# Optimization experiments

Hardware: AMD Instinct MI355X
Metric: run time of the kernel (lower is better)

Reference implementation:

```python
import jax, jax.numpy as jnp
import numpy as np

N = 100000       # num nodes
E = 1600000      # num edges (avg degree 16)
IN, HID, OUT, C = 128, 64, 64, 16


def setup_inputs() -> dict:
    key = jax.random.key(0)
    ks = jax.random.split(key, 10)
    x = jax.random.normal(ks[0], (N, IN), jnp.float32)
    edge_index = jax.random.randint(ks[1], (2, E), 0, N, dtype=jnp.int32)
    dict_node = jax.random.randint(ks[2], (N,), 0, N, dtype=jnp.int32)
    # learned parameters (Glorot-ish scaling)
    W1 = jax.random.normal(ks[3], (IN, HID), jnp.float32) / np.sqrt(IN)
    b1 = jnp.zeros((HID,), jnp.float32)
    W2 = jax.random.normal(ks[4], (HID, OUT), jnp.float32) / np.sqrt(HID)
    b2 = jnp.zeros((OUT,), jnp.float32)
    Wfc = jax.random.normal(ks[5], (OUT, C), jnp.float32) / np.sqrt(OUT)
    bfc = jnp.zeros((C,), jnp.float32)
    return {"x": x, "edge_index": edge_index, "dict_node": dict_node,
            "W1": W1, "b1": b1, "W2": W2, "b2": b2, "Wfc": Wfc, "bfc": bfc}


def _gcn_conv(h_in, W, b, src, dst, n):
    """GCNConv: D^-1/2 (A+I) D^-1/2 (X W) + b, self-loops handled analytically."""
    h = h_in @ W                                   # [N, F]
    deg = jax.ops.segment_sum(jnp.ones((src.shape[0],), h.dtype), dst,
                              num_segments=n) + 1.0  # +1 self-loop
    dinv = jax.lax.rsqrt(deg)                      # [N]
    norm = dinv[src] * dinv[dst]                   # [E]
    agg = jax.ops.segment_sum(h[src] * norm[:, None], dst, num_segments=n)
    agg = agg + h * (dinv * dinv)[:, None]         # self-loop contribution
    return agg + b


def reference(x, edge_index, dict_node, W1, b1, W2, b2, Wfc, bfc):
    n = x.shape[0]
    src, dst = edge_index[0], edge_index[1]
    h = jax.nn.relu(_gcn_conv(x, W1, b1, src, dst, n))
    # dropout p=0.5 is identity at inference
    h = jax.nn.relu(_gcn_conv(h, W2, b2, src, dst, n))
    # global_mean_pool over dict_node with size = num_nodes
    cnt = jax.ops.segment_sum(jnp.ones((n,), h.dtype), dict_node, num_segments=n)
    summ = jax.ops.segment_sum(h, dict_node, num_segments=n)
    pooled = summ / jnp.maximum(cnt, 1.0)[:, None]
    logits = pooled @ Wfc + bfc
    return jax.nn.log_softmax(logits, axis=1)
```

## Files before the change

kernel.cpp:

```cpp
#include <hip/hip_runtime.h>

#define THREADS 256
#define KC 32
#define B1 256

__device__ inline ushort f2bf(float v) {
    union { float f; unsigned u; } a; a.f = v;
    unsigned r = a.u + 0x7fff + ((a.u >> 16) & 1);
    return (ushort)(r >> 16);
}
__device__ inline unsigned pack2(float a, float b) {
    return (unsigned)f2bf(a) | ((unsigned)f2bf(b) << 16);
}
__device__ inline float bflo(unsigned v) {
    union { unsigned u; float f; } a; a.u = v << 16; return a.f;
}
__device__ inline float bfhi(unsigned v) {
    union { unsigned u; float f; } a; a.u = v & 0xffff0000u; return a.f;
}


__global__ void k_p1(const int* __restrict__ dst, int* __restrict__ pc,
                     int E, int NB, int chunk) {
    __shared__ int hist[512];
    int tid = threadIdx.x, blk = blockIdx.x;
    for (int i = tid; i < NB; i += THREADS) hist[i] = 0;
    __syncthreads();
    int e0 = blk * chunk;
    int e1 = e0 + chunk; if (e1 > E) e1 = E;
    for (int e = e0 + tid; e < e1; e += THREADS)
        atomicAdd(&hist[dst[e] >> 8], 1);
    __syncthreads();
    for (int i = tid; i < NB; i += THREADS) pc[i * B1 + blk] = hist[i];
}

__global__ void k_s1(int* __restrict__ pc, int* __restrict__ bsums, int total) {
    __shared__ int s[1024];
    int t = threadIdx.x;
    int idx = blockIdx.x * 1024 + t;
    int v = (idx < total) ? pc[idx] : 0;
    s[t] = v;
    __syncthreads();
    for (int o = 1; o < 1024; o <<= 1) {
        int x = (t >= (unsigned)o) ? s[t - o] : 0;
        __syncthreads();
        s[t] += x;
        __syncthreads();
    }
    if (idx < total) pc[idx] = s[t] - v;
    if (t == 1023) bsums[blockIdx.x] = s[1023];
}

__global__ void k_s2(int* __restrict__ bsums, int nb) {
    __shared__ int s[128];
    int t = threadIdx.x;
    int v = (t < nb) ? bsums[t] : 0;
    s[t] = v;
    __syncthreads();
    for (int o = 1; o < 128; o <<= 1) {
        int x = (t >= (unsigned)o) ? s[t - o] : 0;
        __syncthreads();
        s[t] += x;
        __syncthreads();
    }
    if (t < nb) bsums[t] = s[t] - v;
}


__global__ void k_p2(const int* __restrict__ src, const int* __restrict__ dst,
                     const int* __restrict__ pc, const int* __restrict__ bsx,
                     unsigned long long* __restrict__ part, int E, int NB, int chunk) {
    __shared__ int cur[512];
    int tid = threadIdx.x, blk = blockIdx.x;
    for (int i = tid; i < NB; i += THREADS) {
        int idx = i * B1 + blk;
        cur[i] = pc[idx] + bsx[idx >> 10];
    }
    __syncthreads();
    int e0 = blk * chunk;
    int e1 = e0 + chunk; if (e1 > E) e1 = E;
    for (int e = e0 + tid; e < e1; e += THREADS) {
        int d = dst[e], sv = src[e];
        int pos = atomicAdd(&cur[d >> 8], 1);
        part[pos] = ((unsigned long long)(unsigned)d << 32) | (unsigned)sv;
    }
}

__global__ void k_p3(const unsigned long long* __restrict__ part,
                     const int* __restrict__ pc, const int* __restrict__ bsx,
                     int* __restrict__ off, float* __restrict__ dinv,
                     int* __restrict__ csr, int E, int NB, int n) {
    __shared__ int hist[256];
    __shared__ int so[256];
    int b = blockIdx.x, t = threadIdx.x;
    int i0 = b * B1, i1 = (b + 1) * B1;
    int base = pc[i0] + bsx[i0 >> 10];
    int end  = (b + 1 < NB) ? (pc[i1] + bsx[i1 >> 10]) : E;
    hist[t] = 0;
    __syncthreads();
    for (int e = base + t; e < end; e += THREADS)
        atomicAdd(&hist[(int)(part[e] >> 32) & 255], 1);
    __syncthreads();
    int h = hist[t];
    so[t] = h;
    __syncthreads();
    for (int o = 1; o < 256; o <<= 1) {
        int x = (t >= (unsigned)o) ? so[t - o] : 0;
        __syncthreads();
        so[t] += x;
        __syncthreads();
    }
    int ex = so[t] - h;
    int node = (b << 8) + t;
    if (node < n) {
        off[node]  = base + ex;
        dinv[node] = rsqrtf((float)h + 1.0f);
        if (node == n - 1) off[n] = E;
    }
    __syncthreads();
    so[t] = base + ex;
    __syncthreads();
    for (int e = base + t; e < end; e += THREADS) {
        unsigned long long p = part[e];
        int pos = atomicAdd(&so[(int)(p >> 32) & 255], 1);
        csr[pos] = (int)(p & 0xffffffffu);
    }
}

__global__ __launch_bounds__(THREADS) void
k_g1(const float* __restrict__ X, const float* __restrict__ W,
     const float* __restrict__ dinv, ushort* __restrict__ C, int n, int fin,
     const int* __restrict__ dict, float* __restrict__ cnt, int nGemm, int nCnt) {
    int tid = threadIdx.x;
    if ((int)blockIdx.x >= nGemm) {
        int stride = nCnt * THREADS;
        for (int i = ((int)blockIdx.x - nGemm) * THREADS + tid; i < n; i += stride)
            atomicAdd(&cnt[dict[i]], 1.0f);
        return;
    }
    __shared__ float Xs[KC][68];
    __shared__ float Ws[KC][64];
    int r0  = blockIdx.x * 64;
    int tx4 = (tid & 15) * 4;
    int ty4 = (tid >> 4) * 4;
    int sxr = tid >> 2, sxk = (tid & 3) * 4;
    int swk = tid >> 4, swc = (tid & 15) * 4;
    int xrow = r0 + sxr; if (xrow >= n) xrow = n - 1;
    const float* xptr = X + (size_t)xrow * fin;
    float4 acc0 = {0,0,0,0}, acc1 = {0,0,0,0}, acc2 = {0,0,0,0}, acc3 = {0,0,0,0};
    for (int kc = 0; kc < fin; kc += KC) {
        float4 xa = *(const float4*)(xptr + kc + sxk);
        float4 xb = *(const float4*)(xptr + kc + 16 + sxk);
        float4 wa = *(const float4*)(W + (size_t)(kc + swk) * 64 + swc);
        float4 wb = *(const float4*)(W + (size_t)(kc + swk + 16) * 64 + swc);
        __syncthreads();
        Xs[sxk + 0][sxr] = xa.x; Xs[sxk + 1][sxr] = xa.y;
        Xs[sxk + 2][sxr] = xa.z; Xs[sxk + 3][sxr] = xa.w;
        Xs[16 + sxk + 0][sxr] = xb.x; Xs[16 + sxk + 1][sxr] = xb.y;
        Xs[16 + sxk + 2][sxr] = xb.z; Xs[16 + sxk + 3][sxr] = xb.w;
        *(float4*)&Ws[swk][swc]      = wa;
        *(float4*)&Ws[swk + 16][swc] = wb;
        __syncthreads();
        #pragma unroll 8
        for (int k = 0; k < KC; ++k) {
            float4 a = *(const float4*)&Xs[k][ty4];
            float4 b = *(const float4*)&Ws[k][tx4];
            acc0.x = fmaf(a.x, b.x, acc0.x); acc0.y = fmaf(a.x, b.y, acc0.y);
            acc0.z = fmaf(a.x, b.z, acc0.z); acc0.w = fmaf(a.x, b.w, acc0.w);
            acc1.x = fmaf(a.y, b.x, acc1.x); acc1.y = fmaf(a.y, b.y, acc1.y);
            acc1.z = fmaf(a.y, b.z, acc1.z); acc1.w = fmaf(a.y, b.w, acc1.w);
            acc2.x = fmaf(a.z, b.x, acc2.x); acc2.y = fmaf(a.z, b.y, acc2.y);
            acc2.z = fmaf(a.z, b.z, acc2.z); acc2.w = fmaf(a.z, b.w, acc2.w);
            acc3.x = fmaf(a.w, b.x, acc3.x); acc3.y = fmaf(a.w, b.y, acc3.y);
            acc3.z = fmaf(a.w, b.z, acc3.z); acc3.w = fmaf(a.w, b.w, acc3.w);
        }
    }
    int row = r0 + ty4;
    #pragma unroll
    for (int r = 0; r < 4; ++r) {
        if (row + r >= n) break;
        float dn = dinv[row + r];
        float4 a = r == 0 ? acc0 : r == 1 ? acc1 : r == 2 ? acc2 : acc3;
        ushort4 o;
        o.x = f2bf(a.x * dn); o.y = f2bf(a.y * dn);
        o.z = f2bf(a.z * dn); o.w = f2bf(a.w * dn);
        *(ushort4*)(C + (size_t)(row + r) * 64 + tx4) = o;
    }
}

__global__ __launch_bounds__(THREADS) void
k_gemm_bf16(const ushort* __restrict__ X, const float* __restrict__ W,
            const float* __restrict__ dinv, ushort* __restrict__ C, int n, int fin) {
    __shared__ float Xs[KC][68];
    __shared__ float Ws[KC][64];
    int tid = threadIdx.x;
    int r0  = blockIdx.x * 64;
    int tx4 = (tid & 15) * 4;
    int ty4 = (tid >> 4) * 4;
    int sxr = tid >> 2, sk8 = (tid & 3) * 8;
    int swk = tid >> 4, swc = (tid & 15) * 4;
    int xrow = r0 + sxr; if (xrow >= n) xrow = n - 1;
    const ushort* xptr = X + (size_t)xrow * fin;
    float4 acc0 = {0,0,0,0}, acc1 = {0,0,0,0}, acc2 = {0,0,0,0}, acc3 = {0,0,0,0};
    for (int kc = 0; kc < fin; kc += KC) {
        uint4 xv = *(const uint4*)(xptr + kc + sk8);
        float4 wa = *(const float4*)(W + (size_t)(kc + swk) * 64 + swc);
        float4 wb = *(const float4*)(W + (size_t)(kc + swk + 16) * 64 + swc);
        __syncthreads();
        Xs[sk8 + 0][sxr] = bflo(xv.x); Xs[sk8 + 1][sxr] = bfhi(xv.x);
        Xs[sk8 + 2][sxr] = bflo(xv.y); Xs[sk8 + 3][sxr] = bfhi(xv.y);
        Xs[sk8 + 4][sxr] = bflo(xv.z); Xs[sk8 + 5][sxr] = bfhi(xv.z);
        Xs[sk8 + 6][sxr] = bflo(xv.w); Xs[sk8 + 7][sxr] = bfhi(xv.w);
        *(float4*)&Ws[swk][swc]      = wa;
        *(float4*)&Ws[swk + 16][swc] = wb;
        __syncthreads();
        #pragma unroll 8
        for (int k = 0; k < KC; ++k) {
            float4 a = *(const float4*)&Xs[k][ty4];
            float4 b = *(const float4*)&Ws[k][tx4];
            acc0.x = fmaf(a.x, b.x, acc0.x); acc0.y = fmaf(a.x, b.y, acc0.y);
            acc0.z = fmaf(a.x, b.z, acc0.z); acc0.w = fmaf(a.x, b.w, acc0.w);
            acc1.x = fmaf(a.y, b.x, acc1.x); acc1.y = fmaf(a.y, b.y, acc1.y);
            acc1.z = fmaf(a.y, b.z, acc1.z); acc1.w = fmaf(a.y, b.w, acc1.w);
            acc2.x = fmaf(a.z, b.x, acc2.x); acc2.y = fmaf(a.z, b.y, acc2.y);
            acc2.z = fmaf(a.z, b.z, acc2.z); acc2.w = fmaf(a.z, b.w, acc2.w);
            acc3.x = fmaf(a.w, b.x, acc3.x); acc3.y = fmaf(a.w, b.y, acc3.y);
            acc3.z = fmaf(a.w, b.z, acc3.z); acc3.w = fmaf(a.w, b.w, acc3.w);
        }
    }
    int row = r0 + ty4;
    #pragma unroll
    for (int r = 0; r < 4; ++r) {
        if (row + r >= n) break;
        float dn = dinv[row + r];
        float4 a = r == 0 ? acc0 : r == 1 ? acc1 : r == 2 ? acc2 : acc3;
        ushort4 o;
        o.x = f2bf(a.x * dn); o.y = f2bf(a.y * dn);
        o.z = f2bf(a.z * dn); o.w = f2bf(a.w * dn);
        *(ushort4*)(C + (size_t)(row + r) * 64 + tx4) = o;
    }
}

__device__ inline void gather_sum8(const ushort* __restrict__ H,
                                   const int* __restrict__ csr,
                                   int node, int j, int end, int g, int q,
                                   float4& R0, float4& R1) {
    float4 A0 = {0,0,0,0}, B0 = {0,0,0,0}, A1 = {0,0,0,0}, B1v = {0,0,0,0};
    if (g == 0) {
        uint4 sv = *(const uint4*)(H + ((size_t)node << 6) + q * 8);
        A0.x += bflo(sv.x); A0.y += bfhi(sv.x); A0.z += bflo(sv.y); A0.w += bfhi(sv.y);
        B0.x += bflo(sv.z); B0.y += bfhi(sv.z); B0.z += bflo(sv.w); B0.w += bfhi(sv.w);
    }
    for (; j + 16 <= end; j += 16) {
        int s0 = csr[j + g];
        int s1 = csr[j + 8 + g];
        uint4 v0 = *(const uint4*)(H + ((size_t)s0 << 6) + q * 8);
        uint4 v1 = *(const uint4*)(H + ((size_t)s1 << 6) + q * 8);
        A0.x += bflo(v0.x); A0.y += bfhi(v0.x); A0.z += bflo(v0.y); A0.w += bfhi(v0.y);
        B0.x += bflo(v0.z); B0.y += bfhi(v0.z); B0.z += bflo(v0.w); B0.w += bfhi(v0.w);
        A1.x += bflo(v1.x); A1.y += bfhi(v1.x); A1.z += bflo(v1.y); A1.w += bfhi(v1.y);
        B1v.x += bflo(v1.z); B1v.y += bfhi(v1.z); B1v.z += bflo(v1.w); B1v.w += bfhi(v1.w);
    }
    if (j + 8 <= end) {
        int s0 = csr[j + g];
        uint4 v0 = *(const uint4*)(H + ((size_t)s0 << 6) + q * 8);
        A0.x += bflo(v0.x); A0.y += bfhi(v0.x); A0.z += bflo(v0.y); A0.w += bfhi(v0.y);
        B0.x += bflo(v0.z); B0.y += bfhi(v0.z); B0.z += bflo(v0.w); B0.w += bfhi(v0.w);
        j += 8;
    }
    if (g < end - j) {
        int s1 = csr[j + g];
        uint4 v1 = *(const uint4*)(H + ((size_t)s1 << 6) + q * 8);
        A1.x += bflo(v1.x); A1.y += bfhi(v1.x); A1.z += bflo(v1.y); A1.w += bfhi(v1.y);
        B1v.x += bflo(v1.z); B1v.y += bfhi(v1.z); B1v.z += bflo(v1.w); B1v.w += bfhi(v1.w);
    }
    R0.x = A0.x + A1.x; R0.y = A0.y + A1.y; R0.z = A0.z + A1.z; R0.w = A0.w + A1.w;
    R1.x = B0.x + B1v.x; R1.y = B0.y + B1v.y; R1.z = B0.z + B1v.z; R1.w = B0.w + B1v.w;
    #pragma unroll
    for (int o = 8; o <= 32; o <<= 1) {
        R0.x += __shfl_xor(R0.x, o); R0.y += __shfl_xor(R0.y, o);
        R0.z += __shfl_xor(R0.z, o); R0.w += __shfl_xor(R0.w, o);
        R1.x += __shfl_xor(R1.x, o); R1.y += __shfl_xor(R1.y, o);
        R1.z += __shfl_xor(R1.z, o); R1.w += __shfl_xor(R1.w, o);
    }
}

__global__ void k_gcn_gather(const ushort* __restrict__ H, const int* __restrict__ csr,
                             const int* __restrict__ off, const float* __restrict__ dinv,
                             const float* __restrict__ b, ushort* __restrict__ out, int n) {
    int t = blockIdx.x * blockDim.x + threadIdx.x;
    int node = t >> 6;
    if (node >= n) return;
    int lane = threadIdx.x & 63;
    int g = lane >> 3, q = lane & 7;
    float4 R0, R1;
    gather_sum8(H, csr, node, off[node], off[node + 1], g, q, R0, R1);
    if (g == 0) {
        float dn = dinv[node];
        float4 b0 = *(const float4*)(b + q * 8);
        float4 b1 = *(const float4*)(b + q * 8 + 4);
        float v0 = R0.x * dn + b0.x, v1 = R0.y * dn + b0.y;
        float v2 = R0.z * dn + b0.z, v3 = R0.w * dn + b0.w;
        float v4 = R1.x * dn + b1.x, v5 = R1.y * dn + b1.y;
        float v6 = R1.z * dn + b1.z, v7 = R1.w * dn + b1.w;
        uint4 o;
        o.x = pack2(v0 > 0.f ? v0 : 0.f, v1 > 0.f ? v1 : 0.f);
        o.y = pack2(v2 > 0.f ? v2 : 0.f, v3 > 0.f ? v3 : 0.f);
        o.z = pack2(v4 > 0.f ? v4 : 0.f, v5 > 0.f ? v5 : 0.f);
        o.w = pack2(v6 > 0.f ? v6 : 0.f, v7 > 0.f ? v7 : 0.f);
        *(uint4*)(out + ((size_t)node << 6) + q * 8) = o;
    }
}

__global__ void k_gcn_gather_fc(const ushort* __restrict__ H, const int* __restrict__ csr,
                                const int* __restrict__ off, const float* __restrict__ dinv,
                                const float* __restrict__ b, const float* __restrict__ Wfc,
                                const int* __restrict__ dict, float* __restrict__ pool16,
                                int n) {
    __shared__ float wt[16 * 65];
    __shared__ float hrow[4][64];
    int tid = threadIdx.x;
    for (int i = tid; i < 64 * 16; i += THREADS) {
        int cc = i >> 4, r = i & 15;
        wt[r * 65 + cc] = Wfc[i];
    }
    __syncthreads();
    int t = blockIdx.x * blockDim.x + tid;
    int node = t >> 6;
    int lane = tid & 63;
    int g = lane >> 3, q = lane & 7;
    int nl = tid >> 6;
    if (node < n) {
        float4 R0, R1;
        gather_sum8(H, csr, node, off[node], off[node + 1], g, q, R0, R1);
        if (g == 0) {
            float dn = dinv[node];
            float4 b0 = *(const float4*)(b + q * 8);
            float4 b1 = *(const float4*)(b + q * 8 + 4);
            float4 v0, v1;
            v0.x = R0.x * dn + b0.x; v0.y = R0.y * dn + b0.y;
            v0.z = R0.z * dn + b0.z; v0.w = R0.w * dn + b0.w;
            v1.x = R1.x * dn + b1.x; v1.y = R1.y * dn + b1.y;
            v1.z = R1.z * dn + b1.z; v1.w = R1.w * dn + b1.w;
            v0.x = v0.x > 0.f ? v0.x : 0.f; v0.y = v0.y > 0.f ? v0.y : 0.f;
            v0.z = v0.z > 0.f ? v0.z : 0.f; v0.w = v0.w > 0.f ? v0.w : 0.f;
            v1.x = v1.x > 0.f ? v1.x : 0.f; v1.y = v1.y > 0.f ? v1.y : 0.f;
            v1.z = v1.z > 0.f ? v1.z : 0.f; v1.w = v1.w > 0.f ? v1.w : 0.f;
            *(float4*)&hrow[nl][q * 8]     = v0;
            *(float4*)&hrow[nl][q * 8 + 4] = v1;
        }
        int g2 = lane >> 4, r = lane & 15;
        float p = 0.f;
        #pragma unroll
        for (int i = 0; i < 16; ++i) {
            int cc = g2 * 16 + i;
            p = fmaf(hrow[nl][cc], wt[r * 65 + cc], p);
        }
        p += __shfl_xor(p, 16);
        p += __shfl_xor(p, 32);
        if (g2 == 0)
            atomicAdd(&pool16[(size_t)dict[node] * 16 + r], p);
    }
}

__global__ void k_final16(const float* __restrict__ pool16, const float* __restrict__ cnt,
                          const float* __restrict__ bfc, float* __restrict__ out, int n) {
    int tid = threadIdx.x;
    int nl = tid >> 4, lane = tid & 15;
    int node = blockIdx.x * 16 + nl;
    if (node >= n) return;
    float inv = 1.0f / fmaxf(cnt[node], 1.0f);
    float acc = pool16[(size_t)node * 16 + lane] * inv + bfc[lane];
    float m = acc;
    for (int o = 8; o; o >>= 1) m = fmaxf(m, __shfl_xor(m, o, 16));
    float ex = __expf(acc - m);
    float s = ex;
    for (int o = 8; o; o >>= 1) s += __shfl_xor(s, o, 16);
    out[(size_t)node * 16 + lane] = acc - m - __logf(s);
}

extern "C" void kernel_launch(void* const* d_in, const int* in_sizes, int n_in,
                              void* d_out, int out_size, void* d_ws, size_t ws_size,
                              hipStream_t stream) {
    const float* x    = (const float*)d_in[0];
    const int*   ei   = (const int*)d_in[1];
    const int*   dict = (const int*)d_in[2];
    const float* W1   = (const float*)d_in[3];
    const float* b1   = (const float*)d_in[4];
    const float* W2   = (const float*)d_in[5];
    const float* b2   = (const float*)d_in[6];
    const float* Wfc  = (const float*)d_in[7];
    const float* bfc  = (const float*)d_in[8];

    const int N  = in_sizes[2];
    const int E  = in_sizes[1] / 2;
    const int IN = in_sizes[0] / N;
    const int* src = ei;
    const int* dst = ei + E;

    ushort* bufA = (ushort*)d_ws;
    ushort* bufB = bufA + (size_t)N * 64;
    unsigned long long* part = (unsigned long long*)bufB;
    float* dinv    = (float*)(bufB + (size_t)N * 64);
    float* cnt     = dinv + N;
    int*   off     = (int*)(cnt + N);
    int*   pcounts = off + (N + 1);
    const int NB     = (N + 255) >> 8;
    const int pcsize = NB * B1;
    int*   bsums   = pcounts + pcsize;
    int*   csr     = bsums + 128;
    float* pool16  = (float*)(csr + E);

    const int gNE   = (N * 64 + THREADS - 1) / THREADS;
    const int gTile = (N + 63) / 64;
    const int gRows = (N + 15) / 16;
    const int nCnt  = 256;
    const int chunk = (E + B1 - 1) / B1;
    const int nS1   = (pcsize + 1023) >> 10;

    hipMemsetAsync(cnt, 0, (size_t)N * sizeof(float), stream);
    hipMemsetAsync(pool16, 0, (size_t)N * 16 * sizeof(float), stream);

    k_p1<<<B1, THREADS, 0, stream>>>(dst, pcounts, E, NB, chunk);
    k_s1<<<nS1, 1024, 0, stream>>>(pcounts, bsums, pcsize);
    k_s2<<<1, 128, 0, stream>>>(bsums, nS1);
    k_p2<<<B1, THREADS, 0, stream>>>(src, dst, pcounts, bsums, part, E, NB, chunk);
    k_p3<<<NB, THREADS, 0, stream>>>(part, pcounts, bsums, off, dinv, csr, E, NB, N);

    k_g1<<<gTile + nCnt, THREADS, 0, stream>>>(x, W1, dinv, bufA, N, IN,
                                               dict, cnt, gTile, nCnt);

    k_gcn_gather<<<gNE, THREADS, 0, stream>>>(bufA, csr, off, dinv, b1, bufB, N);

    k_gemm_bf16<<<gTile, THREADS, 0, stream>>>(bufB, W2, dinv, bufA, N, 64);
    k_gcn_gather_fc<<<gNE, THREADS, 0, stream>>>(bufA, csr, off, dinv, b2, Wfc,
                                                 dict, pool16, N);

    k_final16<<<gRows, THREADS, 0, stream>>>(pool16, cnt, bfc, (float*)d_out, N);
}
```

Baseline: 312.9 us.

## Aggregate neighbor features with MFMA segment-sum over 16-node groups per wavefront

```diff
diff --git a/kernel.cpp b/kernel.cpp
--- a/kernel.cpp
+++ b/kernel.cpp
@@ -3,6 +3,10 @@
 #define THREADS 256
 #define KC 32
 #define B1 256
+
+typedef __attribute__((ext_vector_type(8))) short bf16x8;
+typedef __attribute__((ext_vector_type(4))) float f32x4;
+typedef __attribute__((ext_vector_type(2))) unsigned int u32x2;
 
 __device__ inline ushort f2bf(float v) {
     union { float f; unsigned u; } a; a.f = v;
@@ -65,7 +69,6 @@
     }
     if (t < nb) bsums[t] = s[t] - v;
 }
-
 
 __global__ void k_p2(const int* __restrict__ src, const int* __restrict__ dst,
                      const int* __restrict__ pc, const int* __restrict__ bsx,
@@ -241,125 +244,166 @@
     }
 }
 
-__device__ inline void gather_sum8(const ushort* __restrict__ H,
-                                   const int* __restrict__ csr,
-                                   int node, int j, int end, int g, int q,
-                                   float4& R0, float4& R1) {
-    float4 A0 = {0,0,0,0}, B0 = {0,0,0,0}, A1 = {0,0,0,0}, B1v = {0,0,0,0};
-    if (g == 0) {
-        uint4 sv = *(const uint4*)(H + ((size_t)node << 6) + q * 8);
-        A0.x += bflo(sv.x); A0.y += bfhi(sv.x); A0.z += bflo(sv.y); A0.w += bfhi(sv.y);
-        B0.x += bflo(sv.z); B0.y += bfhi(sv.z); B0.z += bflo(sv.w); B0.w += bfhi(sv.w);
-    }
-    for (; j + 16 <= end; j += 16) {
-        int s0 = csr[j + g];
-        int s1 = csr[j + 8 + g];
-        uint4 v0 = *(const uint4*)(H + ((size_t)s0 << 6) + q * 8);
-        uint4 v1 = *(const uint4*)(H + ((size_t)s1 << 6) + q * 8);
-        A0.x += bflo(v0.x); A0.y += bfhi(v0.x); A0.z += bflo(v0.y); A0.w += bfhi(v0.y);
-        B0.x += bflo(v0.z); B0.y += bfhi(v0.z); B0.z += bflo(v0.w); B0.w += bfhi(v0.w);
-        A1.x += bflo(v1.x); A1.y += bfhi(v1.x); A1.z += bflo(v1.y); A1.w += bfhi(v1.y);
-        B1v.x += bflo(v1.z); B1v.y += bfhi(v1.z); B1v.z += bflo(v1.w); B1v.w += bfhi(v1.w);
-    }
-    if (j + 8 <= end) {
-        int s0 = csr[j + g];
-        uint4 v0 = *(const uint4*)(H + ((size_t)s0 << 6) + q * 8);
-        A0.x += bflo(v0.x); A0.y += bfhi(v0.x); A0.z += bflo(v0.y); A0.w += bfhi(v0.y);
-        B0.x += bflo(v0.z); B0.y += bfhi(v0.z); B0.z += bflo(v0.w); B0.w += bfhi(v0.w);
-        j += 8;
-    }
-    if (g < end - j) {
-        int s1 = csr[j + g];
-        uint4 v1 = *(const uint4*)(H + ((size_t)s1 << 6) + q * 8);
-        A1.x += bflo(v1.x); A1.y += bfhi(v1.x); A1.z += bflo(v1.y); A1.w += bfhi(v1.y);
-        B1v.x += bflo(v1.z); B1v.y += bfhi(v1.z); B1v.z += bflo(v1.w); B1v.w += bfhi(v1.w);
-    }
-    R0.x = A0.x + A1.x; R0.y = A0.y + A1.y; R0.z = A0.z + A1.z; R0.w = A0.w + A1.w;
-    R1.x = B0.x + B1v.x; R1.y = B0.y + B1v.y; R1.z = B0.z + B1v.z; R1.w = B0.w + B1v.w;
+__device__ inline void tr_mfma4(unsigned la, const bf16x8& a,
+                                f32x4& o0, f32x4& o1, f32x4& o2, f32x4& o3) {
+    u32x2 r0, r1, r2, r3, r4, r5, r6, r7;
+    asm volatile(
+        "s_waitcnt lgkmcnt(0)\n\t"
+        "ds_read_b64_tr_b16 %0, %8 offset:0\n\t"
+        "ds_read_b64_tr_b16 %1, %8 offset:512\n\t"
+        "ds_read_b64_tr_b16 %2, %8 offset:1024\n\t"
+        "ds_read_b64_tr_b16 %3, %8 offset:1536\n\t"
+        "ds_read_b64_tr_b16 %4, %8 offset:2048\n\t"
+        "ds_read_b64_tr_b16 %5, %8 offset:2560\n\t"
+        "ds_read_b64_tr_b16 %6, %8 offset:3072\n\t"
+        "ds_read_b64_tr_b16 %7, %8 offset:3584\n\t"
+        "s_waitcnt lgkmcnt(0)"
+        : "=&v"(r0), "=&v"(r1), "=&v"(r2), "=&v"(r3),
+          "=&v"(r4), "=&v"(r5), "=&v"(r6), "=&v"(r7)
+        : "v"(la) : "memory");
+    __builtin_amdgcn_sched_barrier(0);
+    union { u32x2 d[2]; bf16x8 v; } b0, b1, b2, b3;
+    b0.d[0] = r0; b0.d[1] = r1; b1.d[0] = r2; b1.d[1] = r3;
+    b2.d[0] = r4; b2.d[1] = r5; b3.d[0] = r6; b3.d[1] = r7;
+    o0 = __builtin_amdgcn_mfma_f32_16x16x32_bf16(a, b0.v, o0, 0, 0, 0);
+    o1 = __builtin_amdgcn_mfma_f32_16x16x32_bf16(a, b1.v, o1, 0, 0, 0);
+    o2 = __builtin_amdgcn_mfma_f32_16x16x32_bf16(a, b2.v, o2, 0, 0, 0);
+    o3 = __builtin_amdgcn_mfma_f32_16x16x32_bf16(a, b3.v, o3, 0, 0, 0);
+}
+
+template<int LAYER>
+__global__ __launch_bounds__(THREADS) void
+k_agg(const ushort* __restrict__ H, const int* __restrict__ csr,
+      const int* __restrict__ off, const float* __restrict__ dinv,
+      const float* __restrict__ bias, ushort* __restrict__ outB,
+      const float* __restrict__ Wfc, const int* __restrict__ dict,
+      float* __restrict__ pool16, int n) {
+    __shared__ ushort cbuf[4][2048];
+    __shared__ float wt[16 * 65];
+    int tid = threadIdx.x;
+    if (LAYER == 2) {
+        for (int i = tid; i < 64 * 16; i += THREADS) {
+            int cc = i >> 4, r = i & 15;
+            wt[r * 65 + cc] = Wfc[i];
+        }
+        __syncthreads();
+    }
+    int wslot = tid >> 6, lane = tid & 63;
+    int gw = blockIdx.x * 4 + wslot;
+    int n0 = gw << 4;
+    if (n0 >= n) return;
+    int G = lane >> 4, c16 = lane & 15;
+    int g8 = lane >> 3, q = lane & 7;
+    ushort* wbuf = &cbuf[wslot][0];
+    unsigned lbase = (unsigned)(size_t)wbuf;
+    int vm = n - n0; if (vm > 16) vm = 16;
+    int sA = 0, eA = 0;
+    if (c16 < vm) { sA = off[n0 + c16]; eA = off[n0 + c16 + 1]; }
+    int base0   = __shfl(sA, 0);
+    int baseEnd = __shfl(eA, vm - 1);
+    unsigned rng = (unsigned)(eA - sA);
+    int sb0 = (q >> 1) * 512 + (g8 >> 2) * 256 + (g8 & 3) * 16 + (q & 1) * 8;
+    unsigned la = lbase + (unsigned)lane * 8;
+    f32x4 acc0 = {0, 0, 0, 0}, acc1 = acc0, acc2 = acc0, acc3 = acc0;
+
+    uint4 cur[4], nxt[4];
     #pragma unroll
-    for (int o = 8; o <= 32; o <<= 1) {
-        R0.x += __shfl_xor(R0.x, o); R0.y += __shfl_xor(R0.y, o);
-        R0.z += __shfl_xor(R0.z, o); R0.w += __shfl_xor(R0.w, o);
-        R1.x += __shfl_xor(R1.x, o); R1.y += __shfl_xor(R1.y, o);
-        R1.z += __shfl_xor(R1.z, o); R1.w += __shfl_xor(R1.w, o);
-    }
-}
-
-__global__ void k_gcn_gather(const ushort* __restrict__ H, const int* __restrict__ csr,
-                             const int* __restrict__ off, const float* __restrict__ dinv,
-                             const float* __restrict__ b, ushort* __restrict__ out, int n) {
-    int t = blockIdx.x * blockDim.x + threadIdx.x;
-    int node = t >> 6;
-    if (node >= n) return;
-    int lane = threadIdx.x & 63;
-    int g = lane >> 3, q = lane & 7;
-    float4 R0, R1;
-    gather_sum8(H, csr, node, off[node], off[node + 1], g, q, R0, R1);
-    if (g == 0) {
-        float dn = dinv[node];
-        float4 b0 = *(const float4*)(b + q * 8);
-        float4 b1 = *(const float4*)(b + q * 8 + 4);
-        float v0 = R0.x * dn + b0.x, v1 = R0.y * dn + b0.y;
-        float v2 = R0.z * dn + b0.z, v3 = R0.w * dn + b0.w;
-        float v4 = R1.x * dn + b1.x, v5 = R1.y * dn + b1.y;
-        float v6 = R1.z * dn + b1.z, v7 = R1.w * dn + b1.w;
-        uint4 o;
-        o.x = pack2(v0 > 0.f ? v0 : 0.f, v1 > 0.f ? v1 : 0.f);
-        o.y = pack2(v2 > 0.f ? v2 : 0.f, v3 > 0.f ? v3 : 0.f);
-        o.z = pack2(v4 > 0.f ? v4 : 0.f, v5 > 0.f ? v5 : 0.f);
-        o.w = pack2(v6 > 0.f ? v6 : 0.f, v7 > 0.f ? v7 : 0.f);
-        *(uint4*)(out + ((size_t)node << 6) + q * 8) = o;
-    }
-}
-
-__global__ void k_gcn_gather_fc(const ushort* __restrict__ H, const int* __restrict__ csr,
-                                const int* __restrict__ off, const float* __restrict__ dinv,
-                                const float* __restrict__ b, const float* __restrict__ Wfc,
-                                const int* __restrict__ dict, float* __restrict__ pool16,
-                                int n) {
-    __shared__ float wt[16 * 65];
-    __shared__ float hrow[4][64];
-    int tid = threadIdx.x;
-    for (int i = tid; i < 64 * 16; i += THREADS) {
-        int cc = i >> 4, r = i & 15;
-        wt[r * 65 + cc] = Wfc[i];
-    }
-    __syncthreads();
-    int t = blockIdx.x * blockDim.x + tid;
-    int node = t >> 6;
-    int lane = tid & 63;
-    int g = lane >> 3, q = lane & 7;
-    int nl = tid >> 6;
-    if (node < n) {
-        float4 R0, R1;
-        gather_sum8(H, csr, node, off[node], off[node + 1], g, q, R0, R1);
-        if (g == 0) {
-            float dn = dinv[node];
-            float4 b0 = *(const float4*)(b + q * 8);
-            float4 b1 = *(const float4*)(b + q * 8 + 4);
-            float4 v0, v1;
-            v0.x = R0.x * dn + b0.x; v0.y = R0.y * dn + b0.y;
-            v0.z = R0.z * dn + b0.z; v0.w = R0.w * dn + b0.w;
-            v1.x = R1.x * dn + b1.x; v1.y = R1.y * dn + b1.y;
-            v1.z = R1.z * dn + b1.z; v1.w = R1.w * dn + b1.w;
-            v0.x = v0.x > 0.f ? v0.x : 0.f; v0.y = v0.y > 0.f ? v0.y : 0.f;
-            v0.z = v0.z > 0.f ? v0.z : 0.f; v0.w = v0.w > 0.f ? v0.w : 0.f;
-            v1.x = v1.x > 0.f ? v1.x : 0.f; v1.y = v1.y > 0.f ? v1.y : 0.f;
-            v1.z = v1.z > 0.f ? v1.z : 0.f; v1.w = v1.w > 0.f ? v1.w : 0.f;
-            *(float4*)&hrow[nl][q * 8]     = v0;
-            *(float4*)&hrow[nl][q * 8 + 4] = v1;
-        }
-        int g2 = lane >> 4, r = lane & 15;
-        float p = 0.f;
-        #pragma unroll
-        for (int i = 0; i < 16; ++i) {
-            int cc = g2 * 16 + i;
-            p = fmaf(hrow[nl][cc], wt[r * 65 + cc], p);
-        }
-        p += __shfl_xor(p, 16);
-        p += __shfl_xor(p, 32);
-        if (g2 == 0)
-            atomicAdd(&pool16[(size_t)dict[node] * 16 + r], p);
+    for (int it = 0; it < 4; ++it) {
+        uint4 v = {0, 0, 0, 0};
+        int k = it * 8 + g8;
+        if (base0 + k < baseEnd) {
+            int e = csr[base0 + k];
+            v = *(const uint4*)(H + ((size_t)e << 6) + q * 8);
+        }
+        cur[it] = v;
+    }
+    for (int base = base0; base < baseEnd; base += 32) {
+        #pragma unroll
+        for (int it = 0; it < 4; ++it) {
+            uint4 v = {0, 0, 0, 0};
+            int k = base + 32 + it * 8 + g8;
+            if (k < baseEnd) {
+                int e = csr[k];
+                v = *(const uint4*)(H + ((size_t)e << 6) + q * 8);
+            }
+            nxt[it] = v;
+        }
+        #pragma unroll
+        for (int it = 0; it < 4; ++it)
+            *(uint4*)(wbuf + sb0 + it * 64) = cur[it];
+        int kb = base - sA;
+        bf16x8 a;
+        #pragma unroll
+        for (int e2 = 0; e2 < 8; ++e2)
+            a[e2] = ((unsigned)(G * 8 + e2 + kb) < rng) ? (short)0x3F80 : (short)0;
+        tr_mfma4(la, a, acc0, acc1, acc2, acc3);
+        #pragma unroll
+        for (int it = 0; it < 4; ++it) cur[it] = nxt[it];
+    }
+    {
+        #pragma unroll
+        for (int it = 0; it < 4; ++it) {
+            uint4 v = {0, 0, 0, 0};
+            int k = it * 8 + g8;
+            if (it < 2 && k < vm)
+                v = *(const uint4*)(H + ((size_t)(n0 + k) << 6) + q * 8);
+            *(uint4*)(wbuf + sb0 + it * 64) = v;
+        }
+        bf16x8 a;
+        #pragma unroll
+        for (int e2 = 0; e2 < 8; ++e2)
+            a[e2] = ((G * 8 + e2) == c16) ? (short)0x3F80 : (short)0;
+        tr_mfma4(la, a, acc0, acc1, acc2, acc3);
+    }
+    float* hrow = (float*)wbuf;
+    float bv0 = bias[c16], bv1 = bias[c16 + 16],
+          bv2 = bias[c16 + 32], bv3 = bias[c16 + 48];
+    #pragma unroll
+    for (int r = 0; r < 4; ++r) {
+        int rr = G * 4 + r;
+        if (rr < vm) {
+            float dn = dinv[n0 + rr];
+            float v0 = fmaxf(acc0[r] * dn + bv0, 0.f);
+            float v1 = fmaxf(acc1[r] * dn + bv1, 0.f);
+            float v2 = fmaxf(acc2[r] * dn + bv2, 0.f);
+            float v3 = fmaxf(acc3[r] * dn + bv3, 0.f);
+            hrow[rr * 64 + c16]      = v0;
+            hrow[rr * 64 + c16 + 16] = v1;
+            hrow[rr * 64 + c16 + 32] = v2;
+            hrow[rr * 64 + c16 + 48] = v3;
+        }
+    }
+    asm volatile("" ::: "memory");
+    if (LAYER == 1) {
+        int prow = lane >> 2, pseg = lane & 3;
+        if (prow < vm) {
+            const float* hp = hrow + prow * 64 + pseg * 16;
+            float4 f0 = *(const float4*)(hp + 0);
+            float4 f1 = *(const float4*)(hp + 4);
+            float4 f2 = *(const float4*)(hp + 8);
+            float4 f3 = *(const float4*)(hp + 12);
+            uint4 o0, o1;
+            o0.x = pack2(f0.x, f0.y); o0.y = pack2(f0.z, f0.w);
+            o0.z = pack2(f1.x, f1.y); o0.w = pack2(f1.z, f1.w);
+            o1.x = pack2(f2.x, f2.y); o1.y = pack2(f2.z, f2.w);
+            o1.z = pack2(f3.x, f3.y); o1.w = pack2(f3.z, f3.w);
+            ushort* op = outB + ((size_t)(n0 + prow) << 6) + pseg * 16;
+            *(uint4*)(op)     = o0;
+            *(uint4*)(op + 8) = o1;
+        }
+    } else {
+        int r16 = c16;
+        for (int m = 0; m < vm; ++m) {
+            const float* hm = hrow + m * 64 + G * 16;
+            const float* wr = wt + r16 * 65 + G * 16;
+            float p = 0.f;
+            #pragma unroll
+            for (int i = 0; i < 16; ++i) p = fmaf(hm[i], wr[i], p);
+            p += __shfl_xor(p, 16);
+            p += __shfl_xor(p, 32);
+            if (G == 0)
+                atomicAdd(&pool16[(size_t)dict[n0 + m] * 16 + r16], p);
+        }
     }
 }
 
@@ -411,12 +455,12 @@
     int*   csr     = bsums + 128;
     float* pool16  = (float*)(csr + E);
 
-    const int gNE   = (N * 64 + THREADS - 1) / THREADS;
     const int gTile = (N + 63) / 64;
     const int gRows = (N + 15) / 16;
     const int nCnt  = 256;
     const int chunk = (E + B1 - 1) / B1;
     const int nS1   = (pcsize + 1023) >> 10;
+    const int gAgg  = ((N + 15) / 16 + 3) / 4;
 
     hipMemsetAsync(cnt, 0, (size_t)N * sizeof(float), stream);
     hipMemsetAsync(pool16, 0, (size_t)N * 16 * sizeof(float), stream);
@@ -430,11 +474,12 @@
     k_g1<<<gTile + nCnt, THREADS, 0, stream>>>(x, W1, dinv, bufA, N, IN,
                                                dict, cnt, gTile, nCnt);
 
-    k_gcn_gather<<<gNE, THREADS, 0, stream>>>(bufA, csr, off, dinv, b1, bufB, N);
+    k_agg<1><<<gAgg, THREADS, 0, stream>>>(bufA, csr, off, dinv, b1, bufB,
+                                           nullptr, nullptr, nullptr, N);
 
     k_gemm_bf16<<<gTile, THREADS, 0, stream>>>(bufB, W2, dinv, bufA, N, 64);
-    k_gcn_gather_fc<<<gNE, THREADS, 0, stream>>>(bufA, csr, off, dinv, b2, Wfc,
-                                                 dict, pool16, N);
+    k_agg<2><<<gAgg, THREADS, 0, stream>>>(bufA, csr, off, dinv, b2, nullptr,
+                                           Wfc, dict, pool16, N);
 
     k_final16<<<gRows, THREADS, 0, stream>>>(pool16, cnt, bfc, (float*)d_out, N);
 }
```

New measurement: 306.0 us. 2.2% less time.
